# Kernel optimization log

Hardware: AMD Instinct MI355X
Metric: run time of the kernel (lower is better)

Reference implementation:

```python
import math
import jax, jax.numpy as jnp
import numpy as np

B, S, H, NH = 4, 2048, 1024, 16
HD = H // NH  # 64


def _rope_cos_sin(seq_len, dim, base=10000.0):
    # freqs[j] = base^(-2j/dim), angles = outer(t, freqs)
    inv = 1.0 / (base ** (jnp.arange(0, dim, 2, dtype=jnp.float32) / dim))
    t = jnp.arange(seq_len, dtype=jnp.float32)
    ang = jnp.outer(t, inv)  # (S, dim//2)
    return jnp.cos(ang), jnp.sin(ang)


def _apply_rope(x, cos, sin):
    # x: (B, S, NH, HD); pairs are (x[2i], x[2i+1]) per torch view_as_complex on reshape(..., -1, 2)
    xr = x.reshape(*x.shape[:-1], HD // 2, 2)
    x0, x1 = xr[..., 0], xr[..., 1]
    c = cos[None, :, None, :]  # (1, S, 1, HD//2)
    s = sin[None, :, None, :]
    o0 = x0 * c - x1 * s
    o1 = x0 * s + x1 * c
    return jnp.stack([o0, o1], axis=-1).reshape(x.shape)


def setup_inputs() -> dict:
    key = jax.random.key(0)
    ks = jax.random.split(key, 5)
    scale = 1.0 / math.sqrt(H)
    return {
        "x": jax.random.normal(ks[0], (B, S, H), dtype=jnp.float32),
        "wq": jax.random.normal(ks[1], (H, H), dtype=jnp.float32) * scale,
        "wk": jax.random.normal(ks[2], (H, H), dtype=jnp.float32) * scale,
        "wv": jax.random.normal(ks[3], (H, H), dtype=jnp.float32) * scale,
        "wo": jax.random.normal(ks[4], (H, H), dtype=jnp.float32) * scale,
        "attention_mask": jnp.ones((B, S), dtype=jnp.int32),
    }


def reference(x, wq, wk, wv, wo, attention_mask):
    # Linear(bias=False): y = x @ W.T with W shape (out, in)
    q = jnp.einsum('bsh,oh->bso', x, wq).reshape(B, S, NH, HD)
    k = jnp.einsum('bsh,oh->bso', x, wk).reshape(B, S, NH, HD)
    v = jnp.einsum('bsh,oh->bso', x, wv).reshape(B, S, NH, HD)
    cos, sin = _rope_cos_sin(S, HD)
    q = _apply_rope(q, cos, sin)
    k = _apply_rope(k, cos, sin)
    # scores: (B, NH, S, S)
    scores = jnp.einsum('bqhd,bkhd->bhqk', q, k) / math.sqrt(HD)
    mask = attention_mask[:, None, None, :]  # (B,1,1,S)
    scores = jnp.where(mask == 0, -jnp.inf, scores)
    attn = jax.nn.softmax(scores, axis=-1)
    # attn_dropout: eval mode / p=0 -> identity
    out = jnp.einsum('bhqk,bkhd->bqhd', attn, v).reshape(B, S, H)
    return jnp.einsum('bsh,oh->bso', out, wo)
```

## Files before the change

kernel.cpp:

```cpp
#include <hip/hip_runtime.h>
#include <hip/hip_bf16.h>

#define B_   4
#define S_   2048
#define H_   1024
#define NH_  16
#define HD_  64
#define M_   8192
#define K_   1024

using bf16x8 = __bf16 __attribute__((ext_vector_type(8)));
using f32x4  = float __attribute__((ext_vector_type(4)));
using f32x16 = float __attribute__((ext_vector_type(16)));

__device__ inline f32x4 mfma16(bf16x8 a, bf16x8 b, f32x4 c) {
    return __builtin_amdgcn_mfma_f32_16x16x32_bf16(a, b, c, 0, 0, 0);
}
__device__ inline f32x16 mfma32(bf16x8 a, bf16x8 b, f32x16 c) {
    return __builtin_amdgcn_mfma_f32_32x32x16_bf16(a, b, c, 0, 0, 0);
}

__device__ inline unsigned short f2bf(float f) {
    __hip_bfloat16 h = __float2bfloat16(f);
    return *reinterpret_cast<unsigned short*>(&h);
}

__device__ inline unsigned cvt_pk_bf16(float lo, float hi) {
    unsigned r;
    asm("v_cvt_pk_bf16_f32 %0, %1, %2" : "=v"(r) : "v"(lo), "v"(hi));
    return r;
}

__device__ inline void perm32swap(unsigned &a, unsigned &b) {
    asm("v_permlane32_swap_b32 %0, %1" : "+v"(a), "+v"(b));
}

__device__ inline void gload_lds16(const unsigned short* g, unsigned short* l) {
    __builtin_amdgcn_global_load_lds(
        (const __attribute__((address_space(1))) void*)g,
        (__attribute__((address_space(3))) void*)l, 16, 0, 0);
}

#define EXP2F(x) __builtin_amdgcn_exp2f(x)


__global__ __launch_bounds__(256) void prep_convert(
    const float* __restrict__ x,  const float* __restrict__ wq,
    const float* __restrict__ wk, const float* __restrict__ wv,
    const float* __restrict__ wo, unsigned short* __restrict__ ws)
{
    size_t u = (size_t)blockIdx.x * 256 + threadIdx.x;
    const float* src; unsigned short* dst; size_t off;
    if (u < 2097152)      { src = x;  dst = ws;            off = u * 4; }
    else if (u < 2359296) { src = wq; dst = ws + 8388608;  off = (u - 2097152) * 4; }
    else if (u < 2621440) { src = wk; dst = ws + 9437184;  off = (u - 2359296) * 4; }
    else if (u < 2883584) { src = wv; dst = ws + 10485760; off = (u - 2621440) * 4; }
    else                  { src = wo; dst = ws + 11534336; off = (u - 2883584) * 4; }
    float4 v = *reinterpret_cast<const float4*>(src + off);
    ushort4 o;
    o.x = f2bf(v.x); o.y = f2bf(v.y); o.z = f2bf(v.z); o.w = f2bf(v.w);
    *reinterpret_cast<ushort4*>(dst + off) = o;
}

__global__ __launch_bounds__(256) void rope_table(
    float2* __restrict__ ropeb, const int* __restrict__ mask,
    float* __restrict__ biasb)
{
    int idx = blockIdx.x * 256 + threadIdx.x;
    int pos = idx >> 5, i = idx & 31;
    float inv = expf(-(float)(2 * i) * (9.210340371976184f / 64.0f));
    float ang = (float)pos * inv;
    float2 cs; cs.x = cosf(ang); cs.y = sinf(ang);
    ropeb[idx] = cs;
    if (idx < B_ * S_)
        biasb[idx] = mask[idx] ? -12.0f : -__builtin_inff();
}

__global__ __launch_bounds__(256) void gemm_qkv(
    const unsigned short* __restrict__ A,
    const unsigned short* __restrict__ W,
    unsigned short* __restrict__ qbuf, unsigned short* __restrict__ kbuf,
    unsigned short* __restrict__ vtb,
    const float* __restrict__ ropeb)
{
    __shared__ alignas(16) unsigned short Al[128 * 64];
    __shared__ alignas(16) unsigned short Bl[128 * 64];

    const int t = threadIdx.x;
    const int l = t & 63;
    const int w = t >> 6;
    const int lane_r = l & 15, lane_g = l >> 4;
    const int bn = blockIdx.x, bm = blockIdx.y;
    const size_t rowbase = (size_t)bm * 128;
    const int colbase = bn * 128;
    const int wm = (w >> 1) * 64, wn = (w & 1) * 64;
    const int which = colbase >> 10;
    const float scale = (which == 0) ? 0.18033688089184827f : 1.0f;

    const int glrow  = l >> 3;
    const int glslot = (l & 7) ^ glrow;

    f32x4 zero4 = {0.f, 0.f, 0.f, 0.f};
    f32x4 acc[4][4];
#pragma unroll
    for (int a = 0; a < 4; a++)
#pragma unroll
        for (int b2 = 0; b2 < 4; b2++) acc[a][b2] = zero4;

    for (int k0 = 0; k0 < K_; k0 += 64) {
#pragma unroll
        for (int i = 0; i < 4; i++) {
            int rbase = i * 32 + w * 8;
            int row = rbase + glrow;
            gload_lds16(A + (rowbase + row) * K_ + k0 + glslot * 8, &Al[rbase * 64]);
            gload_lds16(W + (size_t)(colbase + row) * K_ + k0 + glslot * 8, &Bl[rbase * 64]);
        }
        __syncthreads();

        bf16x8 af[4][2], bfr[4][2];
#pragma unroll
        for (int mt = 0; mt < 4; mt++)
#pragma unroll
            for (int kk = 0; kk < 2; kk++) {
                int rowa = wm + mt * 16 + lane_r;
                int offa = (rowa * 128 + kk * 64 + lane_g * 16) ^ ((rowa & 7) << 4);
                af[mt][kk] = *reinterpret_cast<const bf16x8*>((const char*)Al + offa);
                int rowb = wn + mt * 16 + lane_r;
                int offb = (rowb * 128 + kk * 64 + lane_g * 16) ^ ((rowb & 7) << 4);
                bfr[mt][kk] = *reinterpret_cast<const bf16x8*>((const char*)Bl + offb);
            }
        if (which <= 1) {
#pragma unroll
            for (int a = 0; a < 4; a++)
#pragma unroll
                for (int b2 = 0; b2 < 4; b2++) {
                    acc[a][b2] = mfma16(bfr[a][0], af[b2][0], acc[a][b2]);
                    acc[a][b2] = mfma16(bfr[a][1], af[b2][1], acc[a][b2]);
                }
        } else {
#pragma unroll
            for (int a = 0; a < 4; a++)
#pragma unroll
                for (int b2 = 0; b2 < 4; b2++) {
                    acc[a][b2] = mfma16(af[a][0], bfr[b2][0], acc[a][b2]);
                    acc[a][b2] = mfma16(af[a][1], bfr[b2][1], acc[a][b2]);
                }
        }
        __syncthreads();
    }

    if (which <= 1) {
        unsigned short* out = which ? kbuf : qbuf;
#pragma unroll
        for (int a = 0; a < 4; a++) {
            int nbase = (colbase & 1023) + wn + a * 16 + 4 * lane_g;
            int h = nbase >> 6, d0 = nbase & 63;
#pragma unroll
            for (int b2 = 0; b2 < 4; b2++) {
                size_t r = rowbase + wm + b2 * 16 + lane_r;
                int bb  = (int)(r >> 11);
                int pos = (int)(r & 2047);
                float4 cs = *reinterpret_cast<const float4*>(
                    ropeb + pos * 64 + d0);
                float a0 = acc[a][b2][0], a1 = acc[a][b2][1];
                float a2 = acc[a][b2][2], a3 = acc[a][b2][3];
                float o0 = (a0 * cs.x - a1 * cs.y) * scale;
                float o1 = (a0 * cs.y + a1 * cs.x) * scale;
                float o2 = (a2 * cs.z - a3 * cs.w) * scale;
                float o3 = (a2 * cs.w + a3 * cs.z) * scale;
                uint2 o;
                o.x = cvt_pk_bf16(o0, o1);
                o.y = cvt_pk_bf16(o2, o3);
                *reinterpret_cast<uint2*>(
                    out + (((size_t)(bb * NH_ + h)) * S_ + pos) * 64 + d0) = o;
            }
        }
    } else {
#pragma unroll
        for (int a = 0; a < 4; a++)
#pragma unroll
            for (int b2 = 0; b2 < 4; b2++) {
                size_t rr = rowbase + wm + a * 16 + lane_g * 4;
                int n = (colbase & 1023) + wn + b2 * 16 + lane_r;
                int bb  = (int)(rr >> 11);
                int pos = (int)(rr & 2047);
                int h = n >> 6, d = n & 63;
                ushort4 o;
                o.x = f2bf(acc[a][b2][0]); o.y = f2bf(acc[a][b2][1]);
                o.z = f2bf(acc[a][b2][2]); o.w = f2bf(acc[a][b2][3]);
                *reinterpret_cast<ushort4*>(
                    vtb + (((size_t)(bb * NH_ + h)) * 64 + d) * S_ + pos) = o;
            }
    }
}

__global__ __launch_bounds__(256) void gemm_wo(
    const unsigned short* __restrict__ A,
    const unsigned short* __restrict__ W,
    float* __restrict__ out)
{
    __shared__ alignas(16) unsigned short Al[128 * 64];
    __shared__ alignas(16) unsigned short Bl[128 * 64];

    const int t = threadIdx.x;
    const int l = t & 63;
    const int w = t >> 6;
    const int lane_r = l & 15, lane_g = l >> 4;
    const int bn = blockIdx.x, bm = blockIdx.y;
    const size_t rowbase = (size_t)bm * 128;
    const int colbase = bn * 128;
    const int wm = (w >> 1) * 64, wn = (w & 1) * 64;

    const int glrow  = l >> 3;
    const int glslot = (l & 7) ^ glrow;

    f32x4 zero4 = {0.f, 0.f, 0.f, 0.f};
    f32x4 acc[4][4];
#pragma unroll
    for (int a = 0; a < 4; a++)
#pragma unroll
        for (int b2 = 0; b2 < 4; b2++) acc[a][b2] = zero4;

    for (int k0 = 0; k0 < K_; k0 += 64) {
#pragma unroll
        for (int i = 0; i < 4; i++) {
            int rbase = i * 32 + w * 8;
            int row = rbase + glrow;
            gload_lds16(A + (rowbase + row) * K_ + k0 + glslot * 8, &Al[rbase * 64]);
            gload_lds16(W + (size_t)(colbase + row) * K_ + k0 + glslot * 8, &Bl[rbase * 64]);
        }
        __syncthreads();

        bf16x8 af[4][2], bfr[4][2];
#pragma unroll
        for (int mt = 0; mt < 4; mt++)
#pragma unroll
            for (int kk = 0; kk < 2; kk++) {
                int rowa = wm + mt * 16 + lane_r;
                int offa = (rowa * 128 + kk * 64 + lane_g * 16) ^ ((rowa & 7) << 4);
                af[mt][kk] = *reinterpret_cast<const bf16x8*>((const char*)Al + offa);
                int rowb = wn + mt * 16 + lane_r;
                int offb = (rowb * 128 + kk * 64 + lane_g * 16) ^ ((rowb & 7) << 4);
                bfr[mt][kk] = *reinterpret_cast<const bf16x8*>((const char*)Bl + offb);
            }
#pragma unroll
        for (int mt = 0; mt < 4; mt++)
#pragma unroll
            for (int nt = 0; nt < 4; nt++) {
                acc[mt][nt] = mfma16(af[mt][0], bfr[nt][0], acc[mt][nt]);
                acc[mt][nt] = mfma16(af[mt][1], bfr[nt][1], acc[mt][nt]);
            }
        __syncthreads();
    }

#pragma unroll
    for (int mt = 0; mt < 4; mt++)
#pragma unroll
        for (int nt = 0; nt < 4; nt++)
#pragma unroll
            for (int i = 0; i < 4; i++) {
                size_t r = rowbase + wm + mt * 16 + lane_g * 4 + i;
                int n = colbase + wn + nt * 16 + lane_r;
                out[r * 1024 + n] = acc[mt][nt][i];
            }
}

__global__ __launch_bounds__(256, 2) void attn_fwd(
    const unsigned short* __restrict__ qb, const unsigned short* __restrict__ kb,
    const unsigned short* __restrict__ vt, const float* __restrict__ biasb,
    unsigned short* __restrict__ ao)
{
    __shared__ alignas(16) unsigned short Kl[2][64 * 64];
    __shared__ alignas(16) unsigned short Vl[2][64 * 64];

    const int bid = blockIdx.x;
    const int xcd = bid & 7, idx = bid >> 3;
    const int bh = xcd * 8 + (idx >> 3);
    const int qt = idx & 7;
    const int b = bh >> 4, h = bh & 15;

    const int t = threadIdx.x, l = t & 63, w = t >> 6;
    const int lr = l & 31;
    const int hi = l >> 5;
    const int row8 = lr & 7;

    const unsigned short* qp = qb + (size_t)bh * S_ * 64;
    const unsigned short* kp = kb + (size_t)bh * S_ * 64;
    const unsigned short* vp = vt + (size_t)bh * 64 * S_;
    const float* bp = biasb + (size_t)b * S_;

    bf16x8 qf[2][4];
#pragma unroll
    for (int qbk = 0; qbk < 2; qbk++) {
        int qrow = qt * 256 + w * 64 + qbk * 32 + lr;
#pragma unroll
        for (int ks = 0; ks < 4; ks++)
            qf[qbk][ks] = *reinterpret_cast<const bf16x8*>(
                qp + (size_t)qrow * 64 + ks * 16 + hi * 8);
    }

    f32x16 oacc[2][2];
#pragma unroll
    for (int qbk = 0; qbk < 2; qbk++)
#pragma unroll
        for (int r = 0; r < 16; r++) { oacc[qbk][0][r] = 0.f; oacc[qbk][1][r] = 0.f; }
    float lsum[2] = {0.f, 0.f};

    const int grr = l >> 3;
    const int gss = ((l & 7) ^ grr) * 8;

#define STAGE(bi, kt)                                                          \
    {                                                                          \
        _Pragma("unroll")                                                      \
        for (int c = 0; c < 2; c++) {                                          \
            int rbase = w * 16 + c * 8;                                        \
            gload_lds16(kp + (size_t)((kt) * 64 + rbase + grr) * 64 + gss,     \
                        &Kl[bi][rbase * 64]);                                  \
            gload_lds16(vp + (size_t)(rbase + grr) * S_ + (kt) * 64 + gss,     \
                        &Vl[bi][rbase * 64]);                                  \
        }                                                                      \
    }

#define LOADBIAS(kt)                                                           \
    {                                                                          \
        _Pragma("unroll")                                                      \
        for (int T = 0; T < 2; T++)                                            \
            _Pragma("unroll")                                                  \
            for (int g = 0; g < 4; g++)                                        \
                bvreg[T * 4 + g] = *reinterpret_cast<const float4*>(           \
                    bp + (kt) * 64 + T * 32 + g * 8 + hi * 4);                 \
    }

    float4 bvreg[8];
    STAGE(0, 0)
    LOADBIAS(0)

    for (int kt = 0; kt < 32; kt++) {
        const int cur = kt & 1;
        __syncthreads();
        if (kt < 31) STAGE(cur ^ 1, kt + 1)

        f32x16 sacc[2][2];
#pragma unroll
        for (int T = 0; T < 2; T++)
#pragma unroll
            for (int g = 0; g < 4; g++) {
                float4 bv = bvreg[T * 4 + g];
                sacc[0][T][g * 4 + 0] = bv.x; sacc[0][T][g * 4 + 1] = bv.y;
                sacc[0][T][g * 4 + 2] = bv.z; sacc[0][T][g * 4 + 3] = bv.w;
                sacc[1][T][g * 4 + 0] = bv.x; sacc[1][T][g * 4 + 1] = bv.y;
                sacc[1][T][g * 4 + 2] = bv.z; sacc[1][T][g * 4 + 3] = bv.w;
            }
        if (kt < 31) LOADBIAS(kt + 1)

        __builtin_amdgcn_s_setprio(1);
#pragma unroll
        for (int T = 0; T < 2; T++) {
            int rowb = (32 * T + lr) * 128;
#pragma unroll
            for (int ks = 0; ks < 4; ks++) {
                bf16x8 kf = *reinterpret_cast<const bf16x8*>(
                    (const char*)Kl[cur] + rowb + (((2 * ks + hi) ^ row8) << 4));
                sacc[0][T] = mfma32(kf, qf[0][ks], sacc[0][T]);
                sacc[1][T] = mfma32(kf, qf[1][ks], sacc[1][T]);
            }
        }
        __builtin_amdgcn_s_setprio(0);

        bf16x8 pa[2][4];
#pragma unroll
        for (int qbk = 0; qbk < 2; qbk++) {
            unsigned u[2][8];
            float r0 = 0.f, r1 = 0.f, r2 = 0.f, r3 = 0.f;
#pragma unroll
            for (int T = 0; T < 2; T++) {
                float p[16];
#pragma unroll
                for (int r = 0; r < 16; r++) p[r] = EXP2F(sacc[qbk][T][r]);
#pragma unroll
                for (int r = 0; r < 16; r += 4) {
                    r0 += p[r]; r1 += p[r + 1]; r2 += p[r + 2]; r3 += p[r + 3];
                }
#pragma unroll
                for (int bq = 0; bq < 4; bq++) {
                    u[T][bq * 2 + 0] = cvt_pk_bf16(p[bq * 4 + 0], p[bq * 4 + 1]);
                    u[T][bq * 2 + 1] = cvt_pk_bf16(p[bq * 4 + 2], p[bq * 4 + 3]);
                }
            }
            lsum[qbk] += (r0 + r1) + (r2 + r3);
#pragma unroll
            for (int ks = 0; ks < 4; ks++) {
                int T = ks >> 1, e = ks & 1;
                unsigned a0 = u[T][4 * e + 0], b0 = u[T][4 * e + 2];
                unsigned a1 = u[T][4 * e + 1], b1 = u[T][4 * e + 3];
                perm32swap(a0, b0);
                perm32swap(a1, b1);
                unsigned q4[4] = {a0, a1, b0, b1};
                pa[qbk][ks] = *reinterpret_cast<const bf16x8*>(q4);
            }
        }

        __builtin_amdgcn_s_setprio(1);
#pragma unroll
        for (int dt = 0; dt < 2; dt++) {
            int rowb = (32 * dt + lr) * 128;
#pragma unroll
            for (int ks = 0; ks < 4; ks++) {
                bf16x8 vf = *reinterpret_cast<const bf16x8*>(
                    (const char*)Vl[cur] + rowb + (((2 * ks + hi) ^ row8) << 4));
                oacc[0][dt] = mfma32(vf, pa[0][ks], oacc[0][dt]);
                oacc[1][dt] = mfma32(vf, pa[1][ks], oacc[1][dt]);
            }
        }
        __builtin_amdgcn_s_setprio(0);
    }
#undef STAGE
#undef LOADBIAS

#pragma unroll
    for (int qbk = 0; qbk < 2; qbk++) {
        float ls = lsum[qbk];
        ls += __shfl_xor(ls, 32);
        float rl = 1.0f / ls;
        size_t obase = ((size_t)(b * S_) + qt * 256 + w * 64 + qbk * 32 + lr) * 1024 + h * 64;
#pragma unroll
        for (int dt = 0; dt < 2; dt++)
#pragma unroll
            for (int g = 0; g < 4; g++) {
                uint2 o;
                o.x = cvt_pk_bf16(oacc[qbk][dt][g * 4 + 0] * rl, oacc[qbk][dt][g * 4 + 1] * rl);
                o.y = cvt_pk_bf16(oacc[qbk][dt][g * 4 + 2] * rl, oacc[qbk][dt][g * 4 + 3] * rl);
                *reinterpret_cast<uint2*>(ao + obase + 32 * dt + 8 * g + 4 * hi) = o;
            }
    }
}

extern "C" void kernel_launch(void* const* d_in, const int* in_sizes, int n_in,
                              void* d_out, int out_size, void* d_ws, size_t ws_size,
                              hipStream_t stream)
{
    const float* x  = (const float*)d_in[0];
    const float* wq = (const float*)d_in[1];
    const float* wk = (const float*)d_in[2];
    const float* wv = (const float*)d_in[3];
    const float* wo = (const float*)d_in[4];
    const int* mask = (const int*)d_in[5];

    unsigned short* ws   = (unsigned short*)d_ws;
    unsigned short* xb   = ws;
    unsigned short* wqkv = ws + 8388608;
    unsigned short* wob  = ws + 11534336;
    unsigned short* qbuf = ws + 12582912;
    unsigned short* kbuf = ws + 20971520;
    unsigned short* vtb  = ws + 29360128;
    float* ropeb = (float*)(ws + 37748736);
    float* biasb = (float*)(ws + 38010880);
    unsigned short* aob = xb;

    prep_convert<<<12288, 256, 0, stream>>>(x, wq, wk, wv, wo, ws);
    rope_table<<<256, 256, 0, stream>>>((float2*)ropeb, mask, biasb);

    gemm_qkv<<<dim3(24, 64), 256, 0, stream>>>(xb, wqkv, qbuf, kbuf, vtb, ropeb);

    attn_fwd<<<512, 256, 0, stream>>>(qbuf, kbuf, vtb, biasb, aob);

    gemm_wo<<<dim3(8, 64), 256, 0, stream>>>(aob, wob, (float*)d_out);
}
```

Measured before the change: 203.8 us.

## Double-buffer GEMM LDS tiles with interleaved prefetch and merge QKV/WO kernels

Merges the QKV and output-projection GEMMs into one templated kernel and gives it double-buffered LDS. The next K-tile's global-to-LDS loads are split into chunks and interleaved with quarter-sized MFMA phases under raised wave priority, so memory latency hides behind compute. It also sets launch bounds to 2 blocks per CU and removes bias register prefetching in attention, loading the bias directly each iteration. The cost is twice the LDS per block and extra barriers per K step.

New measurement: 199.4 us. 2.2% less time.

```diff
diff --git a/kernel.cpp b/kernel.cpp
--- a/kernel.cpp
+++ b/kernel.cpp
@@ -76,15 +76,16 @@
         biasb[idx] = mask[idx] ? -12.0f : -__builtin_inff();
 }
 
-__global__ __launch_bounds__(256) void gemm_qkv(
+template<int MODE>
+__global__ __launch_bounds__(256, 2) void gemm_main(
     const unsigned short* __restrict__ A,
     const unsigned short* __restrict__ W,
     unsigned short* __restrict__ qbuf, unsigned short* __restrict__ kbuf,
-    unsigned short* __restrict__ vtb,
+    unsigned short* __restrict__ vtb, float* __restrict__ fout,
     const float* __restrict__ ropeb)
 {
-    __shared__ alignas(16) unsigned short Al[128 * 64];
-    __shared__ alignas(16) unsigned short Bl[128 * 64];
+    __shared__ alignas(16) unsigned short Al[2][128 * 64];
+    __shared__ alignas(16) unsigned short Bl[2][128 * 64];
 
     const int t = threadIdx.x;
     const int l = t & 63;
@@ -94,11 +95,46 @@
     const size_t rowbase = (size_t)bm * 128;
     const int colbase = bn * 128;
     const int wm = (w >> 1) * 64, wn = (w & 1) * 64;
-    const int which = colbase >> 10;
+    const int which = (MODE == 0) ? (colbase >> 10) : 3;
     const float scale = (which == 0) ? 0.18033688089184827f : 1.0f;
 
     const int glrow  = l >> 3;
     const int glslot = (l & 7) ^ glrow;
+    const unsigned short* ga = A + (rowbase + w * 8 + glrow) * K_ + glslot * 8;
+    const unsigned short* gb = W + (size_t)(colbase + w * 8 + glrow) * K_ + glslot * 8;
+
+#define GLA(bi, kt, i) gload_lds16(ga + (size_t)(i) * 32 * K_ + (kt) * 64, \
+                                   &Al[bi][((i) * 32 + w * 8) * 64]);
+#define GLB(bi, kt, i) gload_lds16(gb + (size_t)(i) * 32 * K_ + (kt) * 64, \
+                                   &Bl[bi][((i) * 32 + w * 8) * 64]);
+#define RDA(mt, kk) { int rowa = wm + (mt) * 16 + lane_r;                      \
+    af[mt][kk] = *reinterpret_cast<const bf16x8*>((const char*)Al[cur] +       \
+        ((rowa * 128 + (kk) * 64 + lane_g * 16) ^ ((rowa & 7) << 4))); }
+#define RDB(nt, kk) { int rowb = wn + (nt) * 16 + lane_r;                      \
+    bfr[nt][kk] = *reinterpret_cast<const bf16x8*>((const char*)Bl[cur] +      \
+        ((rowb * 128 + (kk) * 64 + lane_g * 16) ^ ((rowb & 7) << 4))); }
+#define MM(mb, nb)                                                             \
+    if (MODE == 0 && which <= 1) {                                             \
+        _Pragma("unroll")                                                      \
+        for (int a = (nb); a < (nb) + 2; a++)                                  \
+            _Pragma("unroll")                                                  \
+            for (int b2 = (mb); b2 < (mb) + 2; b2++) {                         \
+                acc[a][b2] = mfma16(bfr[a][0], af[b2][0], acc[a][b2]);         \
+                acc[a][b2] = mfma16(bfr[a][1], af[b2][1], acc[a][b2]);         \
+            }                                                                  \
+    } else {                                                                   \
+        _Pragma("unroll")                                                      \
+        for (int mt = (mb); mt < (mb) + 2; mt++)                               \
+            _Pragma("unroll")                                                  \
+            for (int nt = (nb); nt < (nb) + 2; nt++) {                         \
+                acc[mt][nt] = mfma16(af[mt][0], bfr[nt][0], acc[mt][nt]);      \
+                acc[mt][nt] = mfma16(af[mt][1], bfr[nt][1], acc[mt][nt]);      \
+            }                                                                  \
+    }
+#define BARS __builtin_amdgcn_s_barrier();                                     \
+             asm volatile("s_waitcnt lgkmcnt(0)" ::: "memory");                \
+             __builtin_amdgcn_s_setprio(1);
+#define BARE __builtin_amdgcn_s_setprio(0); __builtin_amdgcn_s_barrier();
 
     f32x4 zero4 = {0.f, 0.f, 0.f, 0.f};
     f32x4 acc[4][4];
@@ -107,49 +143,51 @@
 #pragma unroll
         for (int b2 = 0; b2 < 4; b2++) acc[a][b2] = zero4;
 
-    for (int k0 = 0; k0 < K_; k0 += 64) {
-#pragma unroll
-        for (int i = 0; i < 4; i++) {
-            int rbase = i * 32 + w * 8;
-            int row = rbase + glrow;
-            gload_lds16(A + (rowbase + row) * K_ + k0 + glslot * 8, &Al[rbase * 64]);
-            gload_lds16(W + (size_t)(colbase + row) * K_ + k0 + glslot * 8, &Bl[rbase * 64]);
-        }
-        __syncthreads();
-
+    GLA(0, 0, 0) GLA(0, 0, 1) GLA(0, 0, 2) GLA(0, 0, 3)
+    GLB(0, 0, 0) GLB(0, 0, 1) GLB(0, 0, 2) GLB(0, 0, 3)
+    __syncthreads();
+
+    for (int kt = 0; kt < 16; kt++) {
+        const int cur = kt & 1, nxt = cur ^ 1;
+        const bool pf = (kt < 15);
         bf16x8 af[4][2], bfr[4][2];
+        RDA(0, 0) RDA(0, 1) RDA(1, 0) RDA(1, 1)
+        RDB(0, 0) RDB(0, 1) RDB(1, 0) RDB(1, 1)
+        if (pf) { GLA(nxt, kt + 1, 0) GLA(nxt, kt + 1, 1) GLA(nxt, kt + 1, 2) }
+        BARS MM(0, 0) BARE
+        RDB(2, 0) RDB(2, 1) RDB(3, 0) RDB(3, 1)
+        if (pf) { GLA(nxt, kt + 1, 3) GLB(nxt, kt + 1, 0) GLB(nxt, kt + 1, 1) }
+        BARS MM(0, 2) BARE
+        RDA(2, 0) RDA(2, 1) RDA(3, 0) RDA(3, 1)
+        if (pf) { GLB(nxt, kt + 1, 2) GLB(nxt, kt + 1, 3) }
+        BARS MM(2, 2) BARE
+        __builtin_amdgcn_s_setprio(1);
+        MM(2, 0)
+        __builtin_amdgcn_s_setprio(0);
+        asm volatile("s_waitcnt vmcnt(0)" ::: "memory");
+        __builtin_amdgcn_s_barrier();
+    }
+#undef GLA
+#undef GLB
+#undef RDA
+#undef RDB
+#undef MM
+#undef BARS
+#undef BARE
+
+    if (MODE == 1) {
+        float* out = fout;
 #pragma unroll
         for (int mt = 0; mt < 4; mt++)
 #pragma unroll
-            for (int kk = 0; kk < 2; kk++) {
-                int rowa = wm + mt * 16 + lane_r;
-                int offa = (rowa * 128 + kk * 64 + lane_g * 16) ^ ((rowa & 7) << 4);
-                af[mt][kk] = *reinterpret_cast<const bf16x8*>((const char*)Al + offa);
-                int rowb = wn + mt * 16 + lane_r;
-                int offb = (rowb * 128 + kk * 64 + lane_g * 16) ^ ((rowb & 7) << 4);
-                bfr[mt][kk] = *reinterpret_cast<const bf16x8*>((const char*)Bl + offb);
-            }
-        if (which <= 1) {
-#pragma unroll
-            for (int a = 0; a < 4; a++)
-#pragma unroll
-                for (int b2 = 0; b2 < 4; b2++) {
-                    acc[a][b2] = mfma16(bfr[a][0], af[b2][0], acc[a][b2]);
-                    acc[a][b2] = mfma16(bfr[a][1], af[b2][1], acc[a][b2]);
+            for (int nt = 0; nt < 4; nt++)
+#pragma unroll
+                for (int i = 0; i < 4; i++) {
+                    size_t r = rowbase + wm + mt * 16 + lane_g * 4 + i;
+                    int n = colbase + wn + nt * 16 + lane_r;
+                    out[r * 1024 + n] = acc[mt][nt][i];
                 }
-        } else {
-#pragma unroll
-            for (int a = 0; a < 4; a++)
-#pragma unroll
-                for (int b2 = 0; b2 < 4; b2++) {
-                    acc[a][b2] = mfma16(af[a][0], bfr[b2][0], acc[a][b2]);
-                    acc[a][b2] = mfma16(af[a][1], bfr[b2][1], acc[a][b2]);
-                }
-        }
-        __syncthreads();
-    }
-
-    if (which <= 1) {
+    } else if (which <= 1) {
         unsigned short* out = which ? kbuf : qbuf;
 #pragma unroll
         for (int a = 0; a < 4; a++) {
@@ -194,77 +232,6 @@
     }
 }
 
-__global__ __launch_bounds__(256) void gemm_wo(
-    const unsigned short* __restrict__ A,
-    const unsigned short* __restrict__ W,
-    float* __restrict__ out)
-{
-    __shared__ alignas(16) unsigned short Al[128 * 64];
-    __shared__ alignas(16) unsigned short Bl[128 * 64];
-
-    const int t = threadIdx.x;
-    const int l = t & 63;
-    const int w = t >> 6;
-    const int lane_r = l & 15, lane_g = l >> 4;
-    const int bn = blockIdx.x, bm = blockIdx.y;
-    const size_t rowbase = (size_t)bm * 128;
-    const int colbase = bn * 128;
-    const int wm = (w >> 1) * 64, wn = (w & 1) * 64;
-
-    const int glrow  = l >> 3;
-    const int glslot = (l & 7) ^ glrow;
-
-    f32x4 zero4 = {0.f, 0.f, 0.f, 0.f};
-    f32x4 acc[4][4];
-#pragma unroll
-    for (int a = 0; a < 4; a++)
-#pragma unroll
-        for (int b2 = 0; b2 < 4; b2++) acc[a][b2] = zero4;
-
-    for (int k0 = 0; k0 < K_; k0 += 64) {
-#pragma unroll
-        for (int i = 0; i < 4; i++) {
-            int rbase = i * 32 + w * 8;
-            int row = rbase + glrow;
-            gload_lds16(A + (rowbase + row) * K_ + k0 + glslot * 8, &Al[rbase * 64]);
-            gload_lds16(W + (size_t)(colbase + row) * K_ + k0 + glslot * 8, &Bl[rbase * 64]);
-        }
-        __syncthreads();
-
-        bf16x8 af[4][2], bfr[4][2];
-#pragma unroll
-        for (int mt = 0; mt < 4; mt++)
-#pragma unroll
-            for (int kk = 0; kk < 2; kk++) {
-                int rowa = wm + mt * 16 + lane_r;
-                int offa = (rowa * 128 + kk * 64 + lane_g * 16) ^ ((rowa & 7) << 4);
-                af[mt][kk] = *reinterpret_cast<const bf16x8*>((const char*)Al + offa);
-                int rowb = wn + mt * 16 + lane_r;
-                int offb = (rowb * 128 + kk * 64 + lane_g * 16) ^ ((rowb & 7) << 4);
-                bfr[mt][kk] = *reinterpret_cast<const bf16x8*>((const char*)Bl + offb);
-            }
-#pragma unroll
-        for (int mt = 0; mt < 4; mt++)
-#pragma unroll
-            for (int nt = 0; nt < 4; nt++) {
-                acc[mt][nt] = mfma16(af[mt][0], bfr[nt][0], acc[mt][nt]);
-                acc[mt][nt] = mfma16(af[mt][1], bfr[nt][1], acc[mt][nt]);
-            }
-        __syncthreads();
-    }
-
-#pragma unroll
-    for (int mt = 0; mt < 4; mt++)
-#pragma unroll
-        for (int nt = 0; nt < 4; nt++)
-#pragma unroll
-            for (int i = 0; i < 4; i++) {
-                size_t r = rowbase + wm + mt * 16 + lane_g * 4 + i;
-                int n = colbase + wn + nt * 16 + lane_r;
-                out[r * 1024 + n] = acc[mt][nt][i];
-            }
-}
-
 __global__ __launch_bounds__(256, 2) void attn_fwd(
     const unsigned short* __restrict__ qb, const unsigned short* __restrict__ kb,
     const unsigned short* __restrict__ vt, const float* __restrict__ biasb,
@@ -321,19 +288,7 @@
         }                                                                      \
     }
 
-#define LOADBIAS(kt)                                                           \
-    {                                                                          \
-        _Pragma("unroll")                                                      \
-        for (int T = 0; T < 2; T++)                                            \
-            _Pragma("unroll")                                                  \
-            for (int g = 0; g < 4; g++)                                        \
-                bvreg[T * 4 + g] = *reinterpret_cast<const float4*>(           \
-                    bp + (kt) * 64 + T * 32 + g * 8 + hi * 4);                 \
-    }
-
-    float4 bvreg[8];
     STAGE(0, 0)
-    LOADBIAS(0)
 
     for (int kt = 0; kt < 32; kt++) {
         const int cur = kt & 1;
@@ -342,16 +297,17 @@
 
         f32x16 sacc[2][2];
 #pragma unroll
-        for (int T = 0; T < 2; T++)
+        for (int T = 0; T < 2; T++) {
 #pragma unroll
             for (int g = 0; g < 4; g++) {
-                float4 bv = bvreg[T * 4 + g];
+                float4 bv = *reinterpret_cast<const float4*>(
+                    bp + kt * 64 + T * 32 + g * 8 + hi * 4);
                 sacc[0][T][g * 4 + 0] = bv.x; sacc[0][T][g * 4 + 1] = bv.y;
                 sacc[0][T][g * 4 + 2] = bv.z; sacc[0][T][g * 4 + 3] = bv.w;
                 sacc[1][T][g * 4 + 0] = bv.x; sacc[1][T][g * 4 + 1] = bv.y;
                 sacc[1][T][g * 4 + 2] = bv.z; sacc[1][T][g * 4 + 3] = bv.w;
             }
-        if (kt < 31) LOADBIAS(kt + 1)
+        }
 
         __builtin_amdgcn_s_setprio(1);
 #pragma unroll
@@ -415,7 +371,6 @@
         __builtin_amdgcn_s_setprio(0);
     }
 #undef STAGE
-#undef LOADBIAS
 
 #pragma unroll
     for (int qbk = 0; qbk < 2; qbk++) {
@@ -460,9 +415,11 @@
     prep_convert<<<12288, 256, 0, stream>>>(x, wq, wk, wv, wo, ws);
     rope_table<<<256, 256, 0, stream>>>((float2*)ropeb, mask, biasb);
 
-    gemm_qkv<<<dim3(24, 64), 256, 0, stream>>>(xb, wqkv, qbuf, kbuf, vtb, ropeb);
+    gemm_main<0><<<dim3(24, 64), 256, 0, stream>>>(
+        xb, wqkv, qbuf, kbuf, vtb, nullptr, ropeb);
 
     attn_fwd<<<512, 256, 0, stream>>>(qbuf, kbuf, vtb, biasb, aob);
 
-    gemm_wo<<<dim3(8, 64), 256, 0, stream>>>(aob, wob, (float*)d_out);
-}
+    gemm_main<1><<<dim3(8, 64), 256, 0, stream>>>(
+        aob, wob, nullptr, nullptr, nullptr, (float*)d_out, nullptr);
+}
```
